# Kernel tuning notes

Hardware: AMD Instinct MI355X
Metric: run time of the kernel (lower is better)

The kernel has to match this reference:

```python
import jax, jax.numpy as jnp
import numpy as np
import math

B, S, D, H, L = 16, 1024, 256, 8, 4
OBS, ACT = 160, 96
DH = D // H  # 32, even as required by RoPE
ROPE_BASE = 10000.0
LN_EPS = 1e-5


def setup_inputs() -> dict:
    key = jax.random.key(0)
    ks = jax.random.split(key, 16)
    s = 0.02
    n = jax.random.normal
    return {
        "obs_seq": n(ks[0], (B, S, OBS), jnp.float32),
        "action_seq": n(ks[1], (B, S, ACT), jnp.float32),
        # linears stored as [in, out] (transpose of torch convention)
        "in_W": n(ks[2], (OBS + ACT, D), jnp.float32) * s,
        "in_b": jnp.zeros((D,), jnp.float32),
        "qW": n(ks[3], (L, D, D), jnp.float32) * s,
        "qb": jnp.zeros((L, D), jnp.float32),
        "kW": n(ks[4], (L, D, D), jnp.float32) * s,
        "kb": jnp.zeros((L, D), jnp.float32),
        "vW": n(ks[5], (L, D, D), jnp.float32) * s,
        "vb": jnp.zeros((L, D), jnp.float32),
        "oW": n(ks[6], (L, D, D), jnp.float32) * s,
        "ob": jnp.zeros((L, D), jnp.float32),
        "out_W": n(ks[7], (D, D), jnp.float32) * s,
        "out_b": jnp.zeros((D,), jnp.float32),
        "ln_g": jnp.ones((D,), jnp.float32),
        "ln_b": jnp.zeros((D,), jnp.float32),
    }


def _rope(x):
    # x: [B,H,S,DH]; interleaved real/imag rotation (stride-2 split like torch code)
    pos = jnp.arange(S, dtype=jnp.float32)[:, None]                 # [S,1]
    freq_seq = jnp.arange(0, DH, 2, dtype=jnp.float32)              # [DH/2]
    inv_freq = 1.0 / (ROPE_BASE ** (freq_seq / DH))
    freqs = pos * inv_freq[None, :]                                  # [S,DH/2]
    cos = jnp.cos(freqs)[None, None]                                 # [1,1,S,DH/2]
    sin = jnp.sin(freqs)[None, None]
    xr = x[..., 0::2]
    xi = x[..., 1::2]
    rr = xr * cos - xi * sin
    ri = xr * sin + xi * cos
    # interleave back: [..., DH/2, 2] -> [..., DH]
    return jnp.stack([rr, ri], axis=-1).reshape(x.shape)


def _attn_layer(x, qW, qb, kW, kb, vW, vb, oW, ob):
    def heads(t):
        return t.reshape(B, S, H, DH).transpose(0, 2, 1, 3)  # [B,H,S,DH]
    q = _rope(heads(x @ qW + qb))
    k = _rope(heads(x @ kW + kb))
    v = heads(x @ vW + vb)
    scores = jnp.einsum('bhqd,bhkd->bhqk', q, k) / math.sqrt(DH)
    w = jax.nn.softmax(scores, axis=-1)  # dropout is identity at inference
    o = jnp.einsum('bhqk,bhkd->bhqd', w, v)
    o = o.transpose(0, 2, 1, 3).reshape(B, S, D)
    return o @ oW + ob


def reference(obs_seq, action_seq, in_W, in_b, qW, qb, kW, kb, vW, vb, oW, ob,
              out_W, out_b, ln_g, ln_b):
    x = jnp.concatenate([obs_seq, action_seq], axis=-1) @ in_W + in_b  # [B,S,D]
    for l in range(L):  # residual self-attention stack with RoPE
        x = x + _attn_layer(x, qW[l], qb[l], kW[l], kb[l], vW[l], vb[l], oW[l], ob[l])
    y = x @ out_W + out_b
    mu = jnp.mean(y, axis=-1, keepdims=True)
    var = jnp.mean(jnp.square(y - mu), axis=-1, keepdims=True)
    y = (y - mu) / jnp.sqrt(var + LN_EPS) * ln_g + ln_b
    context_embedding = y[:, -1]       # seq_lengths=None path: last timestep
    sequence_embeddings = y
    return context_embedding, sequence_embeddings
```

## Files before the change

kernel.cpp:

```cpp
#include <hip/hip_runtime.h>
#include <hip/hip_bf16.h>
#include <math.h>

#define B_ 16
#define S_ 1024
#define D_ 256
#define H_ 8
#define L_ 4
#define DH_ 32
#define OBS_ 160
#define ACT_ 96
#define M_ (B_*S_)

typedef __attribute__((ext_vector_type(8)))  short short8v;
typedef __attribute__((ext_vector_type(4)))  short short4v;
typedef __attribute__((ext_vector_type(4)))  float f32x4;
typedef __attribute__((ext_vector_type(4)))  unsigned uint4v;

#define ALPHA_ 0.25507313f

__device__ inline short bf16rne(float x) {
    unsigned u = __builtin_bit_cast(unsigned, x);
    unsigned r = (u + 0x7fffu + ((u >> 16) & 1u)) >> 16;
    return (short)r;
}

#if __has_builtin(__builtin_amdgcn_exp2f)
#define EXP2F(x) __builtin_amdgcn_exp2f(x)
#else
#define EXP2F(x) exp2f(x)
#endif

__device__ inline unsigned cvtpk_bf16(float lo, float hi) {
    unsigned r;
    asm("v_cvt_pk_bf16_f32 %0, %1, %2" : "=v"(r) : "v"(lo), "v"(hi));
    return r;
}

__global__ __launch_bounds__(256) void preproc_k(
    const float* __restrict__ obs, const float* __restrict__ act,
    const float* __restrict__ qW, const float* __restrict__ kW,
    const float* __restrict__ vW, const float* __restrict__ oW,
    const float* __restrict__ outW, const float* __restrict__ inW,
    short* __restrict__ xIn,
    short* __restrict__ WTqkv, short* __restrict__ WTo,
    short* __restrict__ WTf, short* __restrict__ WTin,
    float* __restrict__ cosT2, float* __restrict__ sinT2)
{
    __shared__ float T[64][65];
    const int bid = blockIdx.x;
    const int tid = threadIdx.x;

    if (bid < 288) {
        const int bx = bid & 15, z = bid >> 4;
        const int tr = (bx & 3) * 64, tc = (bx >> 2) * 64;
        const float* src;
        short* dst;
        if (z < 16) {
            int lay = z >> 2, w = z & 3;
            if (w == 0)      { src = qW + lay * 65536; dst = WTqkv + lay * 196608; }
            else if (w == 1) { src = kW + lay * 65536; dst = WTqkv + lay * 196608 + 65536; }
            else if (w == 2) { src = vW + lay * 65536; dst = WTqkv + lay * 196608 + 131072; }
            else             { src = oW + lay * 65536; dst = WTo + lay * 65536; }
        } else if (z == 16) { src = outW; dst = WTf; }
        else                { src = inW;  dst = WTin; }
        #pragma unroll
        for (int it = 0; it < 4; ++it) {
            int r = (tid >> 4) + it * 16, c = (tid & 15) * 4;
            *(float4*)&T[r][c] = *(const float4*)&src[(size_t)(tr + r) * 256 + tc + c];
        }
        __syncthreads();
        #pragma unroll
        for (int it = 0; it < 4; ++it) {
            int n = (tid >> 4) + it * 16, k = (tid & 15) * 4;
            short4v o = {bf16rne(T[k][n]), bf16rne(T[k + 1][n]),
                         bf16rne(T[k + 2][n]), bf16rne(T[k + 3][n])};
            *(short4v*)&dst[(size_t)(tc + n) * 256 + tr + k] = o;
        }
    } else if (bid < 2336) {
        const int idx = ((bid - 288) * 256 + tid) * 8;
        const int row = idx >> 8, col = idx & 255;
        const float* s = (col < OBS_) ? (obs + (size_t)row * OBS_ + col)
                                      : (act + (size_t)row * ACT_ + (col - OBS_));
        const float4 v0 = *(const float4*)s;
        const float4 v1 = *(const float4*)(s + 4);
        short8v o = {bf16rne(v0.x), bf16rne(v0.y), bf16rne(v0.z), bf16rne(v0.w),
                     bf16rne(v1.x), bf16rne(v1.y), bf16rne(v1.z), bf16rne(v1.w)};
        *(short8v*)&xIn[idx] = o;
    } else {
        const int idx = (bid - 2336) * 256 + tid;
        const int i = idx >> 10, s = idx & 1023;
        float invf = powf(10000.0f, -(float)(2 * i) / 32.0f);
        float ang = (float)s * invf;
        float sn, cs;
        sincosf(ang, &sn, &cs);
        cosT2[idx] = cs;
        sinT2[idx] = sn;
    }
}

template<int EPI, int IB>
__global__ __launch_bounds__(512, 4) void gemm_k(
    const short* __restrict__ A, const short* __restrict__ WT,
    const float* __restrict__ bq, const float* __restrict__ bk,
    const float* __restrict__ bv,
    float* __restrict__ xF, short* __restrict__ xB,
    short* __restrict__ Q2, short* __restrict__ K2, short* __restrict__ VT,
    float* __restrict__ yF,
    const float* __restrict__ cosT2, const float* __restrict__ sinT2)
{
    __shared__ short As[2][256 * 32];
    __shared__ short Bs[2][64 * 32];
    const int tid = threadIdx.x;
    const int l = tid & 63;
    const int wid = tid >> 6;
    const int wr = wid >> 1, wc = wid & 1;
    const int bm = blockIdx.x * (IB * 64), bn = blockIdx.y * 64;

    const short* aSrc0 = A + (size_t)(bm + (tid >> 2)) * 256 + (tid & 3) * 8;
    const short* aSrc1 = aSrc0 + 128 * 256;
    const short* bSrc  = WT + (size_t)(bn + ((tid & 255) >> 2)) * 256 + (tid & 3) * 8;

    {
        short8v a0 = *(const short8v*)aSrc0;
        *(short8v*)&As[0][tid * 8] = a0;
        if (IB == 4) {
            short8v a1 = *(const short8v*)aSrc1;
            *(short8v*)&As[0][(tid + 512) * 8] = a1;
        }
        if (tid < 256) {
            short8v b0 = *(const short8v*)bSrc;
            *(short8v*)&Bs[0][tid * 8] = b0;
        }
    }
    __syncthreads();

    f32x4 acc[IB][2];
    #pragma unroll
    for (int i = 0; i < IB; ++i)
        #pragma unroll
        for (int j = 0; j < 2; ++j) acc[i][j] = (f32x4){0.f, 0.f, 0.f, 0.f};

    #pragma unroll
    for (int t = 0; t < 8; ++t) {
        const int cur = t & 1;
        short8v na0, na1, nb;
        if (t < 7) {
            const int k = (t + 1) * 32;
            na0 = *(const short8v*)&aSrc0[k];
            if (IB == 4) na1 = *(const short8v*)&aSrc1[k];
            if (tid < 256) nb = *(const short8v*)&bSrc[k];
        }
        short8v af[IB], bf[2];
        #pragma unroll
        for (int i = 0; i < IB; ++i)
            af[i] = *(const short8v*)&As[cur][(wr * (IB * 16) + i * 16 + (l & 15)) * 32 + (l >> 4) * 8];
        #pragma unroll
        for (int j = 0; j < 2; ++j)
            bf[j] = *(const short8v*)&Bs[cur][(wc * 32 + j * 16 + (l & 15)) * 32 + (l >> 4) * 8];
        #pragma unroll
        for (int i = 0; i < IB; ++i)
            #pragma unroll
            for (int j = 0; j < 2; ++j)
                acc[i][j] = __builtin_amdgcn_mfma_f32_16x16x32_bf16(af[i], bf[j], acc[i][j], 0, 0, 0);
        if (t < 7) {
            const int nxt = cur ^ 1;
            *(short8v*)&As[nxt][tid * 8] = na0;
            if (IB == 4) *(short8v*)&As[nxt][(tid + 512) * 8] = na1;
            if (tid < 256) *(short8v*)&Bs[nxt][tid * 8] = nb;
            __syncthreads();
        }
    }

    if (EPI == 0) {
        const int region = bn >> 8;
        if (region != 1) {
            #pragma unroll
            for (int i = 0; i < IB; ++i) {
                const int m0 = bm + wr * (IB * 16) + i * 16 + ((l >> 4) << 2);
                const int bI = m0 >> 10, s0 = m0 & 1023;
                int sp = s0;
                if (region == 2) {
                    const int w = s0 & 31;
                    sp = (s0 & ~31) | ((((w & 15) >> 2) << 3) | ((w >> 4) << 2));
                }
                #pragma unroll
                for (int j = 0; j < 2; ++j) {
                    const int nl = (bn & 255) + wc * 32 + j * 16 + (l & 15);
                    const float bb = (region == 2) ? bv[nl] : bq[nl];
                    f32x4 v = acc[i][j];
                    v[0] += bb; v[1] += bb; v[2] += bb; v[3] += bb;
                    if (region == 0) {
                        v *= ALPHA_;
                        const int ir = (nl & 31) >> 1;
                        const f32x4 cs = *(const f32x4*)&cosT2[ir * 1024 + s0];
                        const f32x4 sn = *(const f32x4*)&sinT2[ir * 1024 + s0];
                        f32x4 pr;
                        #pragma unroll
                        for (int c = 0; c < 4; ++c) pr[c] = __shfl_xor(v[c], 1);
                        const float sg = (nl & 1) ? 1.f : -1.f;
                        #pragma unroll
                        for (int c = 0; c < 4; ++c)
                            v[c] = v[c] * cs[c] + sg * pr[c] * sn[c];
                    }
                    const int h = nl >> 5, dhh = nl & 31;
                    short4v o = {bf16rne(v[0]), bf16rne(v[1]),
                                 bf16rne(v[2]), bf16rne(v[3])};
                    short* dst = (region == 2) ? VT : Q2;
                    *(short4v*)&dst[((size_t)((bI * 8 + h) * 32 + dhh) << 10) + sp] = o;
                }
            }
        } else {
            __syncthreads();
            short* scr = &As[0][0];
            #pragma unroll
            for (int i = 0; i < IB; ++i) {
                const int tl0 = wr * (IB * 16) + i * 16 + ((l >> 4) << 2);
                const int s0r = (bm + tl0) & 1023;
                #pragma unroll
                for (int j = 0; j < 2; ++j) {
                    const int ncl = wc * 32 + j * 16 + (l & 15);
                    const int nl = (bn & 255) + ncl;
                    const float bb = bk[nl];
                    f32x4 v = acc[i][j];
                    v[0] += bb; v[1] += bb; v[2] += bb; v[3] += bb;
                    const int ir = (nl & 31) >> 1;
                    const f32x4 cs = *(const f32x4*)&cosT2[ir * 1024 + s0r];
                    const f32x4 sn = *(const f32x4*)&sinT2[ir * 1024 + s0r];
                    f32x4 pr;
                    #pragma unroll
                    for (int c = 0; c < 4; ++c) pr[c] = __shfl_xor(v[c], 1);
                    const float sg = (nl & 1) ? 1.f : -1.f;
                    #pragma unroll
                    for (int c = 0; c < 4; ++c)
                        v[c] = v[c] * cs[c] + sg * pr[c] * sn[c];
                    #pragma unroll
                    for (int c = 0; c < 4; ++c) {
                        const int tl = tl0 + c;
                        const int pos = (((ncl >> 3) ^ (tl & 7)) << 3) | (ncl & 7);
                        scr[tl * 64 + pos] = bf16rne(v[c]);
                    }
                }
            }
            __syncthreads();
            const int r = tid >> 1, h2 = tid & 1;
            const int tok = bm + r;
            const int bI = tok >> 10, s0 = tok & 1023;
            const int hh = ((bn & 255) >> 5) + h2;
            short* dst = K2 + ((size_t)((bI * 8 + hh) * 1024 + s0)) * 32;
            #pragma unroll
            for (int k = 0; k < 4; ++k) {
                const int pos = ((h2 * 4 + k) ^ (r & 7)) << 3;
                *(uint4*)&dst[k * 8] = *(const uint4*)&scr[r * 64 + pos];
            }
        }
    } else {
        #pragma unroll
        for (int i = 0; i < IB; ++i) {
            const int m0 = bm + wr * (IB * 16) + i * 16 + ((l >> 4) << 2);
            #pragma unroll
            for (int j = 0; j < 2; ++j) {
                const int nn = bn + wc * 32 + j * 16 + (l & 15);
                const float bb = bq[nn];
                const f32x4 v = acc[i][j];
                #pragma unroll
                for (int c = 0; c < 4; ++c) {
                    float rr = v[c] + bb;
                    const size_t off = (size_t)(m0 + c) * 256 + nn;
                    if (EPI == 1) rr += xF[off];
                    if (EPI == 3) {
                        yF[off] = rr;
                    } else {
                        xF[off] = rr;
                        xB[off] = bf16rne(rr);
                    }
                }
            }
        }
    }
}

__global__ __launch_bounds__(512, 2) void attn_k(
    const short* __restrict__ Q2, const short* __restrict__ K2,
    const short* __restrict__ VT, short* __restrict__ O)
{
    __shared__ short lb[65536];
    const int tid = threadIdx.x;
    const int l = tid & 63, wid = tid >> 6;
    const int head = blockIdx.x & 127;
    const int qh = blockIdx.x >> 7;
    const int q0w = qh * 512 + wid * 64;
    const int lq = l & 15, g = l >> 4;

    const short* Kh = K2 + (size_t)head * 32768;
    const short* Vh = VT + (size_t)head * 32768;

    #pragma unroll
    for (int i = 0; i < 8; ++i) {
        const int c = tid + i * 512;
        short8v kv = *(const short8v*)(Kh + c * 8);
        const int key = c >> 2, dc = c & 3;
        *(short8v*)((char*)lb + key * 64 + ((dc ^ ((key >> 1) & 3)) << 4)) = kv;
        short8v vv = *(const short8v*)(Vh + c * 8);
        const int dh = c >> 7, kc = c & 127;
        *(short8v*)((char*)lb + 65536 + (kc >> 2) * 2048 + dh * 64
                    + (((kc & 3) ^ ((dh >> 1) & 3)) << 4)) = vv;
    }

    const short* qbase = Q2 + (size_t)head * 32768 + q0w + lq;
    short8v QfA, QfB, QfC, QfD;
    #pragma unroll
    for (int j = 0; j < 8; ++j) {
        const size_t off = (size_t)(g * 8 + j) * 1024;
        QfA[j] = qbase[off];
        QfB[j] = qbase[off + 16];
        QfC[j] = qbase[off + 32];
        QfD[j] = qbase[off + 48];
    }
    const short one = (short)0x3F80;
    const short8v OnesF = {one, one, one, one, one, one, one, one};

    const char* LBK = (const char*)lb + lq * 64 + ((g ^ ((lq >> 1) & 3)) << 4);
    const char* LBV = LBK + 65536;

    f32x4 aA0 = {0.f,0.f,0.f,0.f}, aA1 = {0.f,0.f,0.f,0.f};
    f32x4 aB0 = {0.f,0.f,0.f,0.f}, aB1 = {0.f,0.f,0.f,0.f};
    f32x4 aC0 = {0.f,0.f,0.f,0.f}, aC1 = {0.f,0.f,0.f,0.f};
    f32x4 aD0 = {0.f,0.f,0.f,0.f}, aD1 = {0.f,0.f,0.f,0.f};
    f32x4 lA = {0.f,0.f,0.f,0.f}, lB = {0.f,0.f,0.f,0.f};
    f32x4 lC = {0.f,0.f,0.f,0.f}, lD = {0.f,0.f,0.f,0.f};
    const f32x4 z4 = {0.f, 0.f, 0.f, 0.f};

    __syncthreads();

#define QSTEP(QF, A0, A1, LACC) do {                                           \
        f32x4 s0 = __builtin_amdgcn_mfma_f32_16x16x32_bf16(Kf0, QF, z4, 0,0,0);\
        f32x4 s1 = __builtin_amdgcn_mfma_f32_16x16x32_bf16(Kf1, QF, z4, 0,0,0);\
        float p0 = EXP2F(s0[0]), p1 = EXP2F(s0[1]);                            \
        float p2 = EXP2F(s0[2]), p3 = EXP2F(s0[3]);                            \
        float p4 = EXP2F(s1[0]), p5 = EXP2F(s1[1]);                            \
        float p6 = EXP2F(s1[2]), p7 = EXP2F(s1[3]);                            \
        uint4v pv = {cvtpk_bf16(p0, p1), cvtpk_bf16(p2, p3),                   \
                     cvtpk_bf16(p4, p5), cvtpk_bf16(p6, p7)};                  \
        short8v Pf = __builtin_bit_cast(short8v, pv);                          \
        A0 = __builtin_amdgcn_mfma_f32_16x16x32_bf16(Vf0, Pf, A0, 0,0,0);      \
        A1 = __builtin_amdgcn_mfma_f32_16x16x32_bf16(Vf1, Pf, A1, 0,0,0);      \
        LACC = __builtin_amdgcn_mfma_f32_16x16x32_bf16(OnesF, Pf, LACC, 0,0,0);\
    } while (0)

    #pragma unroll 4
    for (int t = 0; t < 32; ++t) {
        const short8v Kf0 = *(const short8v*)(LBK + t * 2048);
        const short8v Kf1 = *(const short8v*)(LBK + t * 2048 + 1024);
        const short8v Vf0 = *(const short8v*)(LBV + t * 2048);
        const short8v Vf1 = *(const short8v*)(LBV + t * 2048 + 1024);
        QSTEP(QfA, aA0, aA1, lA);
        QSTEP(QfB, aB0, aB1, lB);
        QSTEP(QfC, aC0, aC1, lC);
        QSTEP(QfD, aD0, aD1, lD);
    }
#undef QSTEP

    const int bI = head >> 3, hh = head & 7;
    short* op = O + ((size_t)(bI * 1024 + q0w + lq)) * 256 + hh * 32 + g * 4;
#define QOUT(A0, A1, LACC, ROFF) do {                                          \
        const float inv = 1.f / (LACC)[0];                                     \
        short4v o0 = {bf16rne(A0[0] * inv), bf16rne(A0[1] * inv),              \
                      bf16rne(A0[2] * inv), bf16rne(A0[3] * inv)};             \
        short4v o1 = {bf16rne(A1[0] * inv), bf16rne(A1[1] * inv),              \
                      bf16rne(A1[2] * inv), bf16rne(A1[3] * inv)};             \
        *(short4v*)(op + (ROFF) * 256) = o0;                                   \
        *(short4v*)(op + (ROFF) * 256 + 16) = o1;                              \
    } while (0)
    QOUT(aA0, aA1, lA, 0);
    QOUT(aB0, aB1, lB, 16);
    QOUT(aC0, aC1, lC, 32);
    QOUT(aD0, aD1, lD, 48);
#undef QOUT
}

__global__ __launch_bounds__(256) void ln_k(
    const float* __restrict__ y, const float* __restrict__ g,
    const float* __restrict__ bta, float* __restrict__ outp)
{
    const int tid = threadIdx.x;
    const int wave = tid >> 6, lane = tid & 63;
    const int row = blockIdx.x * 4 + wave;
    const int col = lane * 4;
    float4 t = *(const float4*)&y[(size_t)row * 256 + col];
    float sum = t.x + t.y + t.z + t.w;
    float ss  = t.x * t.x + t.y * t.y + t.z * t.z + t.w * t.w;
    #pragma unroll
    for (int off = 32; off; off >>= 1) {
        sum += __shfl_xor(sum, off);
        ss  += __shfl_xor(ss, off);
    }
    float mean = sum * (1.f / 256.f);
    float var  = ss * (1.f / 256.f) - mean * mean;
    float rstd = rsqrtf(var + 1e-5f);
    float4 gv = *(const float4*)&g[col];
    float4 bv = *(const float4*)&bta[col];
    float4 o;
    o.x = (t.x - mean) * rstd * gv.x + bv.x;
    o.y = (t.y - mean) * rstd * gv.y + bv.y;
    o.z = (t.z - mean) * rstd * gv.z + bv.z;
    o.w = (t.w - mean) * rstd * gv.w + bv.w;
    float* seq = outp + B_ * D_;
    *(float4*)&seq[(size_t)row * 256 + col] = o;
    if ((row & (S_ - 1)) == S_ - 1)
        *(float4*)&outp[(size_t)(row >> 10) * 256 + col] = o;
}

extern "C" void kernel_launch(void* const* d_in, const int* in_sizes, int n_in,
                              void* d_out, int out_size, void* d_ws, size_t ws_size,
                              hipStream_t stream)
{
    const float* obs  = (const float*)d_in[0];
    const float* act  = (const float*)d_in[1];
    const float* inW  = (const float*)d_in[2];
    const float* inb  = (const float*)d_in[3];
    const float* qW   = (const float*)d_in[4];
    const float* qb   = (const float*)d_in[5];
    const float* kW   = (const float*)d_in[6];
    const float* kb   = (const float*)d_in[7];
    const float* vW   = (const float*)d_in[8];
    const float* vb   = (const float*)d_in[9];
    const float* oW   = (const float*)d_in[10];
    const float* ob   = (const float*)d_in[11];
    const float* outW = (const float*)d_in[12];
    const float* outb = (const float*)d_in[13];
    const float* lng  = (const float*)d_in[14];
    const float* lnb  = (const float*)d_in[15];
    float* outp = (float*)d_out;

    const size_t MD = (size_t)M_ * D_;
    float* xF    = (float*)d_ws;
    short* xB    = (short*)(xF + MD);
    short* xIn   = xB + MD;
    short* Q2    = xIn + MD;
    short* K2    = Q2 + MD;
    short* VT    = K2 + MD;
    short* Obf   = VT + MD;
    short* WTqkv = Obf + MD;
    short* WTo   = WTqkv + 786432;
    short* WTf   = WTo + 262144;
    short* WTin  = WTf + 65536;
    float* cosT2 = (float*)(WTin + 65536);
    float* sinT2 = cosT2 + 16384;
    float* ybuf  = (float*)Q2;

    preproc_k<<<2400, 256, 0, stream>>>(obs, act, qW, kW, vW, oW, outW, inW,
                                        xIn, WTqkv, WTo, WTf, WTin, cosT2, sinT2);

    gemm_k<2,2><<<dim3(128, 4), 512, 0, stream>>>(xIn, WTin, inb, nullptr, nullptr,
            xF, xB, nullptr, nullptr, nullptr, nullptr, nullptr, nullptr);

    for (int lay = 0; lay < L_; ++lay) {
        gemm_k<0,4><<<dim3(64, 12), 512, 0, stream>>>(xB, WTqkv + lay * 196608,
                qb + lay * 256, kb + lay * 256, vb + lay * 256,
                nullptr, nullptr, Q2, K2, VT, nullptr, cosT2, sinT2);
        attn_k<<<256, 512, 0, stream>>>(Q2, K2, VT, Obf);
        gemm_k<1,2><<<dim3(128, 4), 512, 0, stream>>>(Obf, WTo + lay * 65536,
                ob + lay * 256, nullptr, nullptr, xF, xB,
                nullptr, nullptr, nullptr, nullptr, nullptr, nullptr);
    }

    gemm_k<3,2><<<dim3(128, 4), 512, 0, stream>>>(xB, WTf, outb, nullptr, nullptr,
            nullptr, nullptr, nullptr, nullptr, nullptr, ybuf, nullptr, nullptr);
    ln_k<<<M_ / 4, 256, 0, stream>>>(ybuf, lng, lnb, outp);
}
```

Baseline: 255.4 us.

## Fuse final projection with LayerNorm and compute softmax denominators via VALU sums

After: 260.2 us. No clear change (+1.9%).

```diff
diff --git a/kernel.cpp b/kernel.cpp
--- a/kernel.cpp
+++ b/kernel.cpp
@@ -106,7 +106,6 @@
     const float* __restrict__ bv,
     float* __restrict__ xF, short* __restrict__ xB,
     short* __restrict__ Q2, short* __restrict__ K2, short* __restrict__ VT,
-    float* __restrict__ yF,
     const float* __restrict__ cosT2, const float* __restrict__ sinT2)
 {
     __shared__ short As[2][256 * 32];
@@ -268,14 +267,119 @@
                     float rr = v[c] + bb;
                     const size_t off = (size_t)(m0 + c) * 256 + nn;
                     if (EPI == 1) rr += xF[off];
-                    if (EPI == 3) {
-                        yF[off] = rr;
-                    } else {
-                        xF[off] = rr;
-                        xB[off] = bf16rne(rr);
-                    }
+                    xF[off] = rr;
+                    xB[off] = bf16rne(rr);
                 }
             }
+        }
+    }
+}
+
+__global__ __launch_bounds__(512, 2) void gemmln_k(
+    const short* __restrict__ A, const short* __restrict__ WT,
+    const float* __restrict__ outb, const float* __restrict__ lng,
+    const float* __restrict__ lnb, float* __restrict__ outp)
+{
+    __shared__ short As[2][64 * 32];
+    __shared__ short Bs[2][256 * 32];
+    __shared__ float red[64][2][2];
+    const int tid = threadIdx.x;
+    const int l = tid & 63;
+    const int wid = tid >> 6;
+    const int wr2 = wid >> 1, wc2 = wid & 1;
+    const int lq = l & 15, g = l >> 4;
+    const int bm = blockIdx.x * 64;
+
+    const short* aSrc  = A + (size_t)(bm + ((tid & 255) >> 2)) * 256 + (tid & 3) * 8;
+    const short* bSrc0 = WT + (size_t)(tid >> 2) * 256 + (tid & 3) * 8;
+    const short* bSrc1 = bSrc0 + (size_t)128 * 256;
+
+    if (tid < 256) *(short8v*)&As[0][tid * 8] = *(const short8v*)aSrc;
+    *(short8v*)&Bs[0][tid * 8]         = *(const short8v*)bSrc0;
+    *(short8v*)&Bs[0][(tid + 512) * 8] = *(const short8v*)bSrc1;
+    __syncthreads();
+
+    f32x4 acc[8];
+    #pragma unroll
+    for (int j = 0; j < 8; ++j) acc[j] = (f32x4){0.f, 0.f, 0.f, 0.f};
+
+    #pragma unroll
+    for (int t = 0; t < 8; ++t) {
+        const int cur = t & 1;
+        short8v na, nb0, nb1;
+        if (t < 7) {
+            const int k = (t + 1) * 32;
+            if (tid < 256) na = *(const short8v*)&aSrc[k];
+            nb0 = *(const short8v*)&bSrc0[k];
+            nb1 = *(const short8v*)&bSrc1[k];
+        }
+        const short8v af = *(const short8v*)&As[cur][(wr2 * 16 + lq) * 32 + g * 8];
+        short8v bf[8];
+        #pragma unroll
+        for (int j = 0; j < 8; ++j)
+            bf[j] = *(const short8v*)&Bs[cur][(wc2 * 128 + j * 16 + lq) * 32 + g * 8];
+        #pragma unroll
+        for (int j = 0; j < 8; ++j)
+            acc[j] = __builtin_amdgcn_mfma_f32_16x16x32_bf16(af, bf[j], acc[j], 0, 0, 0);
+        if (t < 7) {
+            const int nxt = cur ^ 1;
+            if (tid < 256) *(short8v*)&As[nxt][tid * 8] = na;
+            *(short8v*)&Bs[nxt][tid * 8]         = nb0;
+            *(short8v*)&Bs[nxt][(tid + 512) * 8] = nb1;
+            __syncthreads();
+        }
+    }
+
+    float rs[4] = {0.f, 0.f, 0.f, 0.f}, rq[4] = {0.f, 0.f, 0.f, 0.f};
+    #pragma unroll
+    for (int j = 0; j < 8; ++j) {
+        const float bb = outb[wc2 * 128 + j * 16 + lq];
+        #pragma unroll
+        for (int c = 0; c < 4; ++c) {
+            float v = acc[j][c] + bb;
+            acc[j][c] = v;
+            rs[c] += v;
+            rq[c] += v * v;
+        }
+    }
+    #pragma unroll
+    for (int off = 1; off <= 8; off <<= 1) {
+        #pragma unroll
+        for (int c = 0; c < 4; ++c) {
+            rs[c] += __shfl_xor(rs[c], off);
+            rq[c] += __shfl_xor(rq[c], off);
+        }
+    }
+    if (lq == 0) {
+        #pragma unroll
+        for (int c = 0; c < 4; ++c) {
+            red[wr2 * 16 + g * 4 + c][wc2][0] = rs[c];
+            red[wr2 * 16 + g * 4 + c][wc2][1] = rq[c];
+        }
+    }
+    __syncthreads();
+    float mean[4], rstd[4];
+    #pragma unroll
+    for (int c = 0; c < 4; ++c) {
+        const int row = wr2 * 16 + g * 4 + c;
+        const float sT = red[row][0][0] + red[row][1][0];
+        const float qT = red[row][0][1] + red[row][1][1];
+        mean[c] = sT * (1.f / 256.f);
+        const float var = qT * (1.f / 256.f) - mean[c] * mean[c];
+        rstd[c] = rsqrtf(var + 1e-5f);
+    }
+    float* seq = outp + B_ * D_;
+    #pragma unroll
+    for (int j = 0; j < 8; ++j) {
+        const int col = wc2 * 128 + j * 16 + lq;
+        const float gv = lng[col], bvv = lnb[col];
+        #pragma unroll
+        for (int c = 0; c < 4; ++c) {
+            const int grow = bm + wr2 * 16 + g * 4 + c;
+            const float o = (acc[j][c] - mean[c]) * rstd[c] * gv + bvv;
+            seq[(size_t)grow * 256 + col] = o;
+            if ((grow & (S_ - 1)) == S_ - 1)
+                outp[(size_t)(grow >> 10) * 256 + col] = o;
         }
     }
 }
@@ -317,8 +421,6 @@
         QfC[j] = qbase[off + 32];
         QfD[j] = qbase[off + 48];
     }
-    const short one = (short)0x3F80;
-    const short8v OnesF = {one, one, one, one, one, one, one, one};
 
     const char* LBK = (const char*)lb + lq * 64 + ((g ^ ((lq >> 1) & 3)) << 4);
     const char* LBV = LBK + 65536;
@@ -327,25 +429,24 @@
     f32x4 aB0 = {0.f,0.f,0.f,0.f}, aB1 = {0.f,0.f,0.f,0.f};
     f32x4 aC0 = {0.f,0.f,0.f,0.f}, aC1 = {0.f,0.f,0.f,0.f};
     f32x4 aD0 = {0.f,0.f,0.f,0.f}, aD1 = {0.f,0.f,0.f,0.f};
-    f32x4 lA = {0.f,0.f,0.f,0.f}, lB = {0.f,0.f,0.f,0.f};
-    f32x4 lC = {0.f,0.f,0.f,0.f}, lD = {0.f,0.f,0.f,0.f};
     const f32x4 z4 = {0.f, 0.f, 0.f, 0.f};
+    float lsA = 0.f, lsB = 0.f, lsC = 0.f, lsD = 0.f;
 
     __syncthreads();
 
-#define QSTEP(QF, A0, A1, LACC) do {                                           \
+#define QSTEP(QF, A0, A1, LS) do {                                             \
         f32x4 s0 = __builtin_amdgcn_mfma_f32_16x16x32_bf16(Kf0, QF, z4, 0,0,0);\
         f32x4 s1 = __builtin_amdgcn_mfma_f32_16x16x32_bf16(Kf1, QF, z4, 0,0,0);\
         float p0 = EXP2F(s0[0]), p1 = EXP2F(s0[1]);                            \
         float p2 = EXP2F(s0[2]), p3 = EXP2F(s0[3]);                            \
         float p4 = EXP2F(s1[0]), p5 = EXP2F(s1[1]);                            \
         float p6 = EXP2F(s1[2]), p7 = EXP2F(s1[3]);                            \
+        LS += ((p0 + p1) + (p2 + p3)) + ((p4 + p5) + (p6 + p7));               \
         uint4v pv = {cvtpk_bf16(p0, p1), cvtpk_bf16(p2, p3),                   \
                      cvtpk_bf16(p4, p5), cvtpk_bf16(p6, p7)};                  \
         short8v Pf = __builtin_bit_cast(short8v, pv);                          \
         A0 = __builtin_amdgcn_mfma_f32_16x16x32_bf16(Vf0, Pf, A0, 0,0,0);      \
         A1 = __builtin_amdgcn_mfma_f32_16x16x32_bf16(Vf1, Pf, A1, 0,0,0);      \
-        LACC = __builtin_amdgcn_mfma_f32_16x16x32_bf16(OnesF, Pf, LACC, 0,0,0);\
     } while (0)
 
     #pragma unroll 4
@@ -354,17 +455,21 @@
         const short8v Kf1 = *(const short8v*)(LBK + t * 2048 + 1024);
         const short8v Vf0 = *(const short8v*)(LBV + t * 2048);
         const short8v Vf1 = *(const short8v*)(LBV + t * 2048 + 1024);
-        QSTEP(QfA, aA0, aA1, lA);
-        QSTEP(QfB, aB0, aB1, lB);
-        QSTEP(QfC, aC0, aC1, lC);
-        QSTEP(QfD, aD0, aD1, lD);
+        QSTEP(QfA, aA0, aA1, lsA);
+        QSTEP(QfB, aB0, aB1, lsB);
+        QSTEP(QfC, aC0, aC1, lsC);
+        QSTEP(QfD, aD0, aD1, lsD);
     }
 #undef QSTEP
 
+    lsA += __shfl_xor(lsA, 16); lsA += __shfl_xor(lsA, 32);
+    lsB += __shfl_xor(lsB, 16); lsB += __shfl_xor(lsB, 32);
+    lsC += __shfl_xor(lsC, 16); lsC += __shfl_xor(lsC, 32);
+    lsD += __shfl_xor(lsD, 16); lsD += __shfl_xor(lsD, 32);
     const int bI = head >> 3, hh = head & 7;
     short* op = O + ((size_t)(bI * 1024 + q0w + lq)) * 256 + hh * 32 + g * 4;
-#define QOUT(A0, A1, LACC, ROFF) do {                                          \
-        const float inv = 1.f / (LACC)[0];                                     \
+#define QOUT(A0, A1, LS, ROFF) do {                                            \
+        const float inv = 1.f / (LS);                                          \
         short4v o0 = {bf16rne(A0[0] * inv), bf16rne(A0[1] * inv),              \
                       bf16rne(A0[2] * inv), bf16rne(A0[3] * inv)};             \
         short4v o1 = {bf16rne(A1[0] * inv), bf16rne(A1[1] * inv),              \
@@ -372,43 +477,11 @@
         *(short4v*)(op + (ROFF) * 256) = o0;                                   \
         *(short4v*)(op + (ROFF) * 256 + 16) = o1;                              \
     } while (0)
-    QOUT(aA0, aA1, lA, 0);
-    QOUT(aB0, aB1, lB, 16);
-    QOUT(aC0, aC1, lC, 32);
-    QOUT(aD0, aD1, lD, 48);
+    QOUT(aA0, aA1, lsA, 0);
+    QOUT(aB0, aB1, lsB, 16);
+    QOUT(aC0, aC1, lsC, 32);
+    QOUT(aD0, aD1, lsD, 48);
 #undef QOUT
-}
-
-__global__ __launch_bounds__(256) void ln_k(
-    const float* __restrict__ y, const float* __restrict__ g,
-    const float* __restrict__ bta, float* __restrict__ outp)
-{
-    const int tid = threadIdx.x;
-    const int wave = tid >> 6, lane = tid & 63;
-    const int row = blockIdx.x * 4 + wave;
-    const int col = lane * 4;
-    float4 t = *(const float4*)&y[(size_t)row * 256 + col];
-    float sum = t.x + t.y + t.z + t.w;
-    float ss  = t.x * t.x + t.y * t.y + t.z * t.z + t.w * t.w;
-    #pragma unroll
-    for (int off = 32; off; off >>= 1) {
-        sum += __shfl_xor(sum, off);
-        ss  += __shfl_xor(ss, off);
-    }
-    float mean = sum * (1.f / 256.f);
-    float var  = ss * (1.f / 256.f) - mean * mean;
-    float rstd = rsqrtf(var + 1e-5f);
-    float4 gv = *(const float4*)&g[col];
-    float4 bv = *(const float4*)&bta[col];
-    float4 o;
-    o.x = (t.x - mean) * rstd * gv.x + bv.x;
-    o.y = (t.y - mean) * rstd * gv.y + bv.y;
-    o.z = (t.z - mean) * rstd * gv.z + bv.z;
-    o.w = (t.w - mean) * rstd * gv.w + bv.w;
-    float* seq = outp + B_ * D_;
-    *(float4*)&seq[(size_t)row * 256 + col] = o;
-    if ((row & (S_ - 1)) == S_ - 1)
-        *(float4*)&outp[(size_t)(row >> 10) * 256 + col] = o;
 }
 
 extern "C" void kernel_launch(void* const* d_in, const int* in_sizes, int n_in,
@@ -447,25 +520,22 @@
     short* WTin  = WTf + 65536;
     float* cosT2 = (float*)(WTin + 65536);
     float* sinT2 = cosT2 + 16384;
-    float* ybuf  = (float*)Q2;
 
     preproc_k<<<2400, 256, 0, stream>>>(obs, act, qW, kW, vW, oW, outW, inW,
                                         xIn, WTqkv, WTo, WTf, WTin, cosT2, sinT2);
 
     gemm_k<2,2><<<dim3(128, 4), 512, 0, stream>>>(xIn, WTin, inb, nullptr, nullptr,
-            xF, xB, nullptr, nullptr, nullptr, nullptr, nullptr, nullptr);
+            xF, xB, nullptr, nullptr, nullptr, nullptr, nullptr);
 
     for (int lay = 0; lay < L_; ++lay) {
         gemm_k<0,4><<<dim3(64, 12), 512, 0, stream>>>(xB, WTqkv + lay * 196608,
                 qb + lay * 256, kb + lay * 256, vb + lay * 256,
-                nullptr, nullptr, Q2, K2, VT, nullptr, cosT2, sinT2);
+                nullptr, nullptr, Q2, K2, VT, cosT2, sinT2);
         attn_k<<<256, 512, 0, stream>>>(Q2, K2, VT, Obf);
         gemm_k<1,2><<<dim3(128, 4), 512, 0, stream>>>(Obf, WTo + lay * 65536,
                 ob + lay * 256, nullptr, nullptr, xF, xB,
-                nullptr, nullptr, nullptr, nullptr, nullptr, nullptr);
-    }
-
-    gemm_k<3,2><<<dim3(128, 4), 512, 0, stream>>>(xB, WTf, outb, nullptr, nullptr,
-            nullptr, nullptr, nullptr, nullptr, nullptr, ybuf, nullptr, nullptr);
-    ln_k<<<M_ / 4, 256, 0, stream>>>(ybuf, lng, lnb, outp);
-}
+                nullptr, nullptr, nullptr, nullptr, nullptr);
+    }
+
+    gemmln_k<<<256, 512, 0, stream>>>(xB, WTf, outb, lng, lnb, outp);
+}
```
